# Optimization experiments

Measured on AMD Instinct MI355X. Metric: run time of the kernel, lower is better.

The kernel has to match this reference:

```python
import jax, jax.numpy as jnp
import numpy as np

N_Q = 4  # QuantumSampler is hard-wired to 4 qubits (16-dim statevector)


def _build_tables():
    """Static permutation for the CNOT chain and Z-sign table, computed once in numpy."""
    n = N_Q
    dim = 1 << n
    cnots = [(i, (i + 1) % n) for i in range(n)]  # (0,1),(1,2),(2,3),(3,0)
    fmap = np.empty(dim, dtype=np.int64)
    for i in range(dim):
        bits = [(i >> (n - 1 - w)) & 1 for w in range(n)]  # wire w <-> bit (n-1-w)
        for c, t in cnots:
            if bits[c]:
                bits[t] ^= 1
        fmap[i] = sum(b << (n - 1 - w) for w, b in enumerate(bits))
    finv = np.argsort(fmap)  # new_state[j] = old_state[finv[j]]
    signs = np.array([[1.0 - 2.0 * ((j >> (n - 1 - w)) & 1) for w in range(n)]
                      for j in range(dim)], dtype=np.float32)  # <Z_w> signs per basis state
    return jnp.asarray(finv), jnp.asarray(signs)

PERM, SIGNS = _build_tables()


def quantum_gate_probs(q, theta):
    """Simulate: RX(q_w) then RX(theta_w) per wire (angles add), CNOT chain, <Z> per wire, softmax.
    q: [B,4] encoder angles; theta: [4] trainable angles. Returns [B,4] gate probabilities."""
    half = 0.5 * (q + theta)                      # RX(a)RX(b) = RX(a+b)
    c = jnp.cos(half).astype(jnp.complex64)       # amplitude on |0>
    s = (jnp.sin(half).astype(jnp.complex64)) * (-1j)  # amplitude on |1> is -i sin(a/2)
    a = jnp.stack([c, s], axis=-1)                # [B,4,2] single-qubit states
    a0, a1, a2, a3 = a[:, 0], a[:, 1], a[:, 2], a[:, 3]
    # product state |psi> = a0 (x) a1 (x) a2 (x) a3  -> [B,2,2,2,2] -> [B,16]
    st = (a0[:, :, None, None, None] * a1[:, None, :, None, None]
          * a2[:, None, None, :, None] * a3[:, None, None, None, :])
    st = st.reshape(q.shape[0], 16)[:, PERM]      # apply CNOT chain (amplitude permutation)
    probs = st.real ** 2 + st.imag ** 2           # [B,16]
    exps = probs @ SIGNS                          # [B,4] Pauli-Z expectations per wire
    return jax.nn.softmax(exps, axis=-1)


def setup_inputs() -> dict:
    key = jax.random.key(0)
    ks = jax.random.split(key, 8)
    T, B, D, H = 256, 128, 1024, 1024
    inputs = jax.random.normal(ks[0], (T, B, D), dtype=jnp.float32)
    sc_d = 1.0 / np.sqrt(D)
    sc_h = 1.0 / np.sqrt(H)
    return {
        "inputs": inputs,
        "Wi": jax.random.normal(ks[1], (H, D), dtype=jnp.float32) * sc_d,
        "bi": jnp.zeros((H,), dtype=jnp.float32),
        "Wh": jax.random.normal(ks[2], (H, H), dtype=jnp.float32) * sc_h,
        "bh": jnp.zeros((H,), dtype=jnp.float32),
        "Wq": jax.random.normal(ks[3], (4, H), dtype=jnp.float32) * sc_h,
        "bq": jnp.zeros((4,), dtype=jnp.float32),
        "theta": jax.random.uniform(ks[4], (4,), dtype=jnp.float32, minval=-np.pi, maxval=np.pi),
    }


def reference(inputs, Wi, bi, Wh, bh, Wq, bq, theta):
    T, B, _ = inputs.shape
    H = Wi.shape[0]
    hx0 = jnp.zeros((B, H), dtype=inputs.dtype)
    cx0 = jnp.zeros((B, H), dtype=inputs.dtype)

    def step(carry, x):
        hx, cx = carry
        combined = x @ Wi.T + bi + hx @ Wh.T + bh   # [B,H]
        qin = combined @ Wq.T + bq                  # [B,4]
        gates = quantum_gate_probs(qin, theta)      # [B,4]
        f, i_, g, o = gates[:, 0:1], gates[:, 1:2], gates[:, 2:3], gates[:, 3:4]
        cx = f * cx + i_ * jnp.tanh(g)              # broadcast [B,1]*[B,H]
        hx = o * jnp.tanh(cx)
        return (hx, cx), hx

    (hx, cx), ys = jax.lax.scan(step, (hx0, cx0), inputs)
    return ys, hx, cx
```

## Files before the change

kernel.cpp:

```cpp
#include <hip/hip_runtime.h>

#define T_STEPS 256
#define BATCH   128
#define DIM     1024
#define NROWS   (T_STEPS * BATCH)
#define TOTROWS (NROWS + 2 * BATCH)

typedef float vfloat4 __attribute__((ext_vector_type(4)));

#define WS_M     0
#define WS_V     4096
#define WS_CB    4128
#define WS_ZERO_BYTES ((WS_CB + 4) * 4)
#define WS_QX    8192
#define WS_HSEQ  (WS_QX + 4 * NROWS)
#define WS_CFIN  (WS_HSEQ + NROWS)

__global__ __launch_bounds__(256) void k_prep(const float* __restrict__ Wi,
                                              const float* __restrict__ Wh,
                                              const float* __restrict__ bi,
                                              const float* __restrict__ bh,
                                              const float* __restrict__ Wq,
                                              float* __restrict__ M,
                                              float* __restrict__ v,
                                              float* __restrict__ cb) {
    int blk  = blockIdx.x;
    int tid  = threadIdx.x;
    int wave = tid >> 6;
    int lane = tid & 63;

    if (blk < 64) {
        int j0 = blk * 16;
        #pragma unroll
        for (int db = 0; db < 4; db++) {
            int d = db * 256 + tid;
            float a0 = 0.f, a1 = 0.f, a2 = 0.f, a3 = 0.f;
            #pragma unroll 4
            for (int jj = 0; jj < 16; jj++) {
                int j = j0 + jj;
                float wv = Wi[(size_t)j * DIM + d];
                a0 += Wq[0 * DIM + j] * wv;
                a1 += Wq[1 * DIM + j] * wv;
                a2 += Wq[2 * DIM + j] * wv;
                a3 += Wq[3 * DIM + j] * wv;
            }
            unsafeAtomicAdd(&M[0 * DIM + d], a0);
            unsafeAtomicAdd(&M[1 * DIM + d], a1);
            unsafeAtomicAdd(&M[2 * DIM + d], a2);
            unsafeAtomicAdd(&M[3 * DIM + d], a3);
        }
    } else {
        int j0 = (blk - 64) * 16 + wave * 4;
        float sv0 = 0.f, sv1 = 0.f, sv2 = 0.f, sv3 = 0.f;
        float sc0 = 0.f, sc1 = 0.f, sc2 = 0.f, sc3 = 0.f;
        #pragma unroll
        for (int jj = 0; jj < 4; jj++) {
            int j = j0 + jj;
            const float4* row = (const float4*)(Wh + (size_t)j * DIM);
            float s = 0.f;
            #pragma unroll
            for (int k = 0; k < 4; k++) {
                float4 t4 = row[k * 64 + lane];
                s += t4.x + t4.y + t4.z + t4.w;
            }
            #pragma unroll
            for (int off = 32; off; off >>= 1) s += __shfl_xor(s, off, 64);
            float bsum = bi[j] + bh[j];
            float q0 = Wq[0 * DIM + j], q1 = Wq[1 * DIM + j];
            float q2 = Wq[2 * DIM + j], q3 = Wq[3 * DIM + j];
            sv0 += q0 * s;    sv1 += q1 * s;    sv2 += q2 * s;    sv3 += q3 * s;
            sc0 += q0 * bsum; sc1 += q1 * bsum; sc2 += q2 * bsum; sc3 += q3 * bsum;
        }
        if (lane == 0) {
            unsafeAtomicAdd(&v[0], sv0);  unsafeAtomicAdd(&v[1], sv1);
            unsafeAtomicAdd(&v[2], sv2);  unsafeAtomicAdd(&v[3], sv3);
            unsafeAtomicAdd(&cb[0], sc0); unsafeAtomicAdd(&cb[1], sc1);
            unsafeAtomicAdd(&cb[2], sc2); unsafeAtomicAdd(&cb[3], sc3);
        }
    }
}

__global__ __launch_bounds__(256) void k_qx(const float* __restrict__ x,
                                            const float* __restrict__ M,
                                            float4* __restrict__ qxT) {
    int gtid   = blockIdx.x * blockDim.x + threadIdx.x;
    int wave   = gtid >> 6;
    int lane   = threadIdx.x & 63;
    int nwaves = (gridDim.x * blockDim.x) >> 6;

    float4 m[4][4];
    #pragma unroll
    for (int w = 0; w < 4; w++)
        #pragma unroll
        for (int k = 0; k < 4; k++)
            m[w][k] = *(const float4*)(M + w * DIM + k * 256 + lane * 4);

    for (int r = wave; r < NROWS; r += nwaves) {
        const float4* row = (const float4*)(x + (size_t)r * DIM);
        float a0 = 0.f, a1 = 0.f, a2 = 0.f, a3 = 0.f;
        #pragma unroll
        for (int k = 0; k < 4; k++) {
            float4 xv = row[k * 64 + lane];
            a0 += xv.x * m[0][k].x + xv.y * m[0][k].y + xv.z * m[0][k].z + xv.w * m[0][k].w;
            a1 += xv.x * m[1][k].x + xv.y * m[1][k].y + xv.z * m[1][k].z + xv.w * m[1][k].w;
            a2 += xv.x * m[2][k].x + xv.y * m[2][k].y + xv.z * m[2][k].z + xv.w * m[2][k].w;
            a3 += xv.x * m[3][k].x + xv.y * m[3][k].y + xv.z * m[3][k].z + xv.w * m[3][k].w;
        }
        #pragma unroll
        for (int off = 32; off; off >>= 1) {
            a0 += __shfl_xor(a0, off, 64);
            a1 += __shfl_xor(a1, off, 64);
            a2 += __shfl_xor(a2, off, 64);
            a3 += __shfl_xor(a3, off, 64);
        }
        if (lane == 0) {
            int t = r >> 7, b = r & 127;
            qxT[(size_t)b * T_STEPS + t] = make_float4(a0, a1, a2, a3);
        }
    }
}

__device__ __forceinline__ float fast_tanh(float x) {
    float e = __expf(2.f * x);
    return (e - 1.f) * __builtin_amdgcn_rcpf(e + 1.f);
}

__device__ __forceinline__ void rec_step(float4 q,
                                         float b0, float b1, float b2, float b3,
                                         float v0, float v1, float v2, float v3,
                                         float& h, float& c) {
    float z0 = __cosf(q.x + b0 + h * v0);
    float z1 = __cosf(q.y + b1 + h * v1);
    float z2 = __cosf(q.z + b2 + h * v2);
    float z3 = __cosf(q.w + b3 + h * v3);
    float e1 = z0 * z1;
    float e2 = e1 * z2;
    float e3 = e2 * z3;
    float e0 = z1 * z2 * z3;
    float x0 = __expf(e0), x1 = __expf(e1), x2 = __expf(e2), x3 = __expf(e3);
    float inv = __builtin_amdgcn_rcpf(x0 + x1 + x2 + x3);
    float f  = x0 * inv;
    float i_ = x1 * inv;
    float g  = x2 * inv;
    float o  = x3 * inv;
    c = f * c + i_ * fast_tanh(g);
    h = o * fast_tanh(c);
}

__global__ __launch_bounds__(128) void k_rec(const float* __restrict__ bq,
                                             const float* __restrict__ theta,
                                             const float* __restrict__ v,
                                             const float* __restrict__ cbp,
                                             const float4* __restrict__ qxT,
                                             float* __restrict__ hT,
                                             float* __restrict__ cfin) {
    int b = threadIdx.x;

    float v0 = v[0], v1 = v[1], v2 = v[2], v3 = v[3];
    float b0 = cbp[0] + bq[0] + theta[0];
    float b1 = cbp[1] + bq[1] + theta[1];
    float b2 = cbp[2] + bq[2] + theta[2];
    float b3 = cbp[3] + bq[3] + theta[3];

    const float4* qrow = qxT + (size_t)b * T_STEPS;
    float4*       hrow = (float4*)(hT + (size_t)b * T_STEPS);

    float h = 0.f, c = 0.f;
    float4 q0 = qrow[0], q1 = qrow[1], q2 = qrow[2], q3 = qrow[3];
    float4 q4 = qrow[4], q5 = qrow[5], q6 = qrow[6], q7 = qrow[7];

    for (int t = 0; t < T_STEPS; t += 8) {
        float4 n0, n1, n2, n3, n4, n5, n6, n7;
        if (t + 8 < T_STEPS) {
            n0 = qrow[t + 8];  n1 = qrow[t + 9];  n2 = qrow[t + 10]; n3 = qrow[t + 11];
            n4 = qrow[t + 12]; n5 = qrow[t + 13]; n6 = qrow[t + 14]; n7 = qrow[t + 15];
        }
        float h0, h1, h2, h3, h4, h5, h6, h7;
        rec_step(q0, b0, b1, b2, b3, v0, v1, v2, v3, h, c); h0 = h;
        rec_step(q1, b0, b1, b2, b3, v0, v1, v2, v3, h, c); h1 = h;
        rec_step(q2, b0, b1, b2, b3, v0, v1, v2, v3, h, c); h2 = h;
        rec_step(q3, b0, b1, b2, b3, v0, v1, v2, v3, h, c); h3 = h;
        rec_step(q4, b0, b1, b2, b3, v0, v1, v2, v3, h, c); h4 = h;
        rec_step(q5, b0, b1, b2, b3, v0, v1, v2, v3, h, c); h5 = h;
        rec_step(q6, b0, b1, b2, b3, v0, v1, v2, v3, h, c); h6 = h;
        rec_step(q7, b0, b1, b2, b3, v0, v1, v2, v3, h, c); h7 = h;
        hrow[(t >> 2) + 0] = make_float4(h0, h1, h2, h3);
        hrow[(t >> 2) + 1] = make_float4(h4, h5, h6, h7);
        q0 = n0; q1 = n1; q2 = n2; q3 = n3; q4 = n4; q5 = n5; q6 = n6; q7 = n7;
    }
    cfin[b] = c;
}

__global__ __launch_bounds__(256) void k_write(const float* __restrict__ hT,
                                               const float* __restrict__ cfin,
                                               float* __restrict__ out) {
    int tid  = threadIdx.x;
    int r    = blockIdx.x * 4 + (tid >> 6);
    int lane = tid & 63;

    float val;
    if      (r < NROWS)          val = hT[(size_t)(r & 127) * T_STEPS + (r >> 7)];
    else if (r < NROWS + BATCH)  val = hT[(size_t)(r - NROWS) * T_STEPS + (T_STEPS - 1)];
    else                         val = cfin[r - NROWS - BATCH];

    vfloat4 vv = {val, val, val, val};
    vfloat4* orow = (vfloat4*)(out + (size_t)r * DIM);
    __builtin_nontemporal_store(vv, &orow[0 * 64 + lane]);
    __builtin_nontemporal_store(vv, &orow[1 * 64 + lane]);
    __builtin_nontemporal_store(vv, &orow[2 * 64 + lane]);
    __builtin_nontemporal_store(vv, &orow[3 * 64 + lane]);
}

extern "C" void kernel_launch(void* const* d_in, const int* in_sizes, int n_in,
                              void* d_out, int out_size, void* d_ws, size_t ws_size,
                              hipStream_t stream) {
    const float* inputs = (const float*)d_in[0];
    const float* Wi     = (const float*)d_in[1];
    const float* bi     = (const float*)d_in[2];
    const float* Wh     = (const float*)d_in[3];
    const float* bh     = (const float*)d_in[4];
    const float* Wq     = (const float*)d_in[5];
    const float* bq     = (const float*)d_in[6];
    const float* theta  = (const float*)d_in[7];
    float* out = (float*)d_out;
    float* ws  = (float*)d_ws;

    float*  M    = ws + WS_M;
    float*  v    = ws + WS_V;
    float*  cb   = ws + WS_CB;
    float4* qxT  = (float4*)(ws + WS_QX);
    float*  hT   = ws + WS_HSEQ;
    float*  cfin = ws + WS_CFIN;

    (void)hipMemsetAsync(ws, 0, WS_ZERO_BYTES, stream);
    k_prep <<<128,  256, 0, stream>>>(Wi, Wh, bi, bh, Wq, M, v, cb);
    k_qx   <<<1024, 256, 0, stream>>>(inputs, M, qxT);
    k_rec  <<<1,    128, 0, stream>>>(bq, theta, v, cb, qxT, hT, cfin);
    k_write<<<TOTROWS / 4, 256, 0, stream>>>(hT, cfin, out);
}
```

Before: 317.9 us.

## Drop memset, move Wh-sum work into qx kernel, rational tanh in recurrence

Removes the workspace memset by having k_prep compute M through a shared-memory reduction instead of atomics, and zero v/cb in an extra block. The Wh row-sum and bias projection moves into extra blocks of k_qx, leaving k_prep with only 17 blocks. The serial recurrence step replaces its exp-based tanh calls with Padé rational approximations to shorten the per-step dependency chain, trading some accuracy for fewer transcendental ops. The k_qx blocks that atomically add into v and cb rely on the zeroing in k_prep having completed first.

Result: slower. 340.3 us (+7.0%).

```diff
diff --git a/kernel.cpp b/kernel.cpp
--- a/kernel.cpp
+++ b/kernel.cpp
@@ -11,46 +11,63 @@
 #define WS_M     0
 #define WS_V     4096
 #define WS_CB    4128
-#define WS_ZERO_BYTES ((WS_CB + 4) * 4)
 #define WS_QX    8192
 #define WS_HSEQ  (WS_QX + 4 * NROWS)
 #define WS_CFIN  (WS_HSEQ + NROWS)
 
 __global__ __launch_bounds__(256) void k_prep(const float* __restrict__ Wi,
-                                              const float* __restrict__ Wh,
-                                              const float* __restrict__ bi,
-                                              const float* __restrict__ bh,
                                               const float* __restrict__ Wq,
                                               float* __restrict__ M,
                                               float* __restrict__ v,
                                               float* __restrict__ cb) {
     int blk  = blockIdx.x;
     int tid  = threadIdx.x;
+    if (blk < 16) {
+        int lane = tid & 63;
+        int jq   = tid >> 6;
+        int d    = blk * 64 + lane;
+        float a0 = 0.f, a1 = 0.f, a2 = 0.f, a3 = 0.f;
+        int j0 = jq * 256;
+        #pragma unroll 4
+        for (int j = j0; j < j0 + 256; j++) {
+            float wv = Wi[(size_t)j * DIM + d];
+            a0 += Wq[0 * DIM + j] * wv;
+            a1 += Wq[1 * DIM + j] * wv;
+            a2 += Wq[2 * DIM + j] * wv;
+            a3 += Wq[3 * DIM + j] * wv;
+        }
+        __shared__ float sm[4][64][4];
+        sm[jq][lane][0] = a0; sm[jq][lane][1] = a1;
+        sm[jq][lane][2] = a2; sm[jq][lane][3] = a3;
+        __syncthreads();
+        if (tid < 64) {
+            #pragma unroll
+            for (int w = 0; w < 4; w++)
+                M[w * DIM + blk * 64 + tid] =
+                    sm[0][tid][w] + sm[1][tid][w] + sm[2][tid][w] + sm[3][tid][w];
+        }
+    } else {
+        if (tid < 4)      v[tid]      = 0.f;
+        else if (tid < 8) cb[tid - 4] = 0.f;
+    }
+}
+
+__global__ __launch_bounds__(256) void k_qx(const float* __restrict__ x,
+                                            const float* __restrict__ Wh,
+                                            const float* __restrict__ bi,
+                                            const float* __restrict__ bh,
+                                            const float* __restrict__ Wq,
+                                            const float* __restrict__ M,
+                                            float4* __restrict__ qxT,
+                                            float* __restrict__ v,
+                                            float* __restrict__ cb) {
+    int blk  = blockIdx.x;
+    int tid  = threadIdx.x;
     int wave = tid >> 6;
     int lane = tid & 63;
 
-    if (blk < 64) {
-        int j0 = blk * 16;
-        #pragma unroll
-        for (int db = 0; db < 4; db++) {
-            int d = db * 256 + tid;
-            float a0 = 0.f, a1 = 0.f, a2 = 0.f, a3 = 0.f;
-            #pragma unroll 4
-            for (int jj = 0; jj < 16; jj++) {
-                int j = j0 + jj;
-                float wv = Wi[(size_t)j * DIM + d];
-                a0 += Wq[0 * DIM + j] * wv;
-                a1 += Wq[1 * DIM + j] * wv;
-                a2 += Wq[2 * DIM + j] * wv;
-                a3 += Wq[3 * DIM + j] * wv;
-            }
-            unsafeAtomicAdd(&M[0 * DIM + d], a0);
-            unsafeAtomicAdd(&M[1 * DIM + d], a1);
-            unsafeAtomicAdd(&M[2 * DIM + d], a2);
-            unsafeAtomicAdd(&M[3 * DIM + d], a3);
-        }
-    } else {
-        int j0 = (blk - 64) * 16 + wave * 4;
+    if (blk >= 1024) {
+        int j0 = (blk - 1024) * 16 + wave * 4;
         float sv0 = 0.f, sv1 = 0.f, sv2 = 0.f, sv3 = 0.f;
         float sc0 = 0.f, sc1 = 0.f, sc2 = 0.f, sc3 = 0.f;
         #pragma unroll
@@ -77,16 +94,8 @@
             unsafeAtomicAdd(&cb[0], sc0); unsafeAtomicAdd(&cb[1], sc1);
             unsafeAtomicAdd(&cb[2], sc2); unsafeAtomicAdd(&cb[3], sc3);
         }
-    }
-}
-
-__global__ __launch_bounds__(256) void k_qx(const float* __restrict__ x,
-                                            const float* __restrict__ M,
-                                            float4* __restrict__ qxT) {
-    int gtid   = blockIdx.x * blockDim.x + threadIdx.x;
-    int wave   = gtid >> 6;
-    int lane   = threadIdx.x & 63;
-    int nwaves = (gridDim.x * blockDim.x) >> 6;
+        return;
+    }
 
     float4 m[4][4];
     #pragma unroll
@@ -95,7 +104,8 @@
         for (int k = 0; k < 4; k++)
             m[w][k] = *(const float4*)(M + w * DIM + k * 256 + lane * 4);
 
-    for (int r = wave; r < NROWS; r += nwaves) {
+    int nwaves = 1024 * 4;
+    for (int r = blk * 4 + wave; r < NROWS; r += nwaves) {
         const float4* row = (const float4*)(x + (size_t)r * DIM);
         float a0 = 0.f, a1 = 0.f, a2 = 0.f, a3 = 0.f;
         #pragma unroll
@@ -118,11 +128,6 @@
             qxT[(size_t)b * T_STEPS + t] = make_float4(a0, a1, a2, a3);
         }
     }
-}
-
-__device__ __forceinline__ float fast_tanh(float x) {
-    float e = __expf(2.f * x);
-    return (e - 1.f) * __builtin_amdgcn_rcpf(e + 1.f);
 }
 
 __device__ __forceinline__ void rec_step(float4 q,
@@ -133,18 +138,25 @@
     float z1 = __cosf(q.y + b1 + h * v1);
     float z2 = __cosf(q.z + b2 + h * v2);
     float z3 = __cosf(q.w + b3 + h * v3);
-    float e1 = z0 * z1;
-    float e2 = e1 * z2;
-    float e3 = e2 * z3;
-    float e0 = z1 * z2 * z3;
-    float x0 = __expf(e0), x1 = __expf(e1), x2 = __expf(e2), x3 = __expf(e3);
-    float inv = __builtin_amdgcn_rcpf(x0 + x1 + x2 + x3);
-    float f  = x0 * inv;
-    float i_ = x1 * inv;
-    float g  = x2 * inv;
-    float o  = x3 * inv;
-    c = f * c + i_ * fast_tanh(g);
-    h = o * fast_tanh(c);
+    float p01 = z0 * z1, p23 = z2 * z3;
+    float x0 = __expf(z1 * p23);
+    float x1 = __expf(p01);
+    float x2 = __expf(p01 * z2);
+    float x3 = __expf(p01 * p23);
+    float S  = (x0 + x1) + (x2 + x3);
+    float x2q = x2 * x2, Sq = S * S;
+    float A = Sq * Sq, B = x2q * Sq, C = x2q * x2q;
+    float Ng = fmaf(945.f, A, fmaf(105.f, B, C));
+    float Dg = fmaf(945.f, A, fmaf(420.f, B, 15.f * C));
+    float SD = S * Dg;
+    float r1 = __builtin_amdgcn_rcpf(Sq * Dg);
+    c = fmaf(x0 * c, SD, (x1 * x2) * Ng) * r1;
+    float cq = c * c;
+    float cq2 = cq * cq;
+    float Nc = fmaf(105.f, cq, 945.f + cq2);
+    float Dc = fmaf(420.f, cq, fmaf(15.f, cq2, 945.f));
+    float r2 = __builtin_amdgcn_rcpf(S * Dc);
+    h = ((x3 * c) * Nc) * r2;
 }
 
 __global__ __launch_bounds__(128) void k_rec(const float* __restrict__ bq,
@@ -232,9 +244,8 @@
     float*  hT   = ws + WS_HSEQ;
     float*  cfin = ws + WS_CFIN;
 
-    (void)hipMemsetAsync(ws, 0, WS_ZERO_BYTES, stream);
-    k_prep <<<128,  256, 0, stream>>>(Wi, Wh, bi, bh, Wq, M, v, cb);
-    k_qx   <<<1024, 256, 0, stream>>>(inputs, M, qxT);
+    k_prep <<<17,   256, 0, stream>>>(Wi, Wq, M, v, cb);
+    k_qx   <<<1088, 256, 0, stream>>>(inputs, Wh, bi, bh, Wq, M, qxT, v, cb);
     k_rec  <<<1,    128, 0, stream>>>(bq, theta, v, cb, qxT, hT, cfin);
     k_write<<<TOTROWS / 4, 256, 0, stream>>>(hT, cfin, out);
 }
```
